# Optimization experiments

Measured on AMD Instinct MI355X. Metric: run time of the kernel, lower is better.

The kernel has to match this reference:

```python
import jax, jax.numpy as jnp
import numpy as np

NUM_CLASSES = 64
BASE_MARGIN = 0.1
ADAPTIVE_WEIGHT = 0.1
STAT_WEIGHT = 0.1


def setup_inputs() -> dict:
    key = jax.random.key(0)
    k1, k2 = jax.random.split(key)
    feats = jax.random.normal(k1, (4096, 512), dtype=jnp.float32)
    labels = jax.random.randint(k2, (4096,), 0, NUM_CLASSES, dtype=jnp.int64)
    return {"feats": feats, "labels": labels}


def _forward(feats, labels):
    N, D = feats.shape
    # pairwise euclidean distances (torch.cdist p=2), nan-safe sqrt
    sq = jnp.sum(feats * feats, axis=-1)                      # [N]
    d2 = sq[:, None] + sq[None, :] - 2.0 * (feats @ feats.T)  # [N,N]
    d2 = jnp.maximum(d2, 0.0)
    dist = jnp.sqrt(jnp.where(d2 > 0.0, d2, 1.0))
    dist = jnp.where(d2 > 0.0, dist, 0.0)

    # class stats (first-call EMA == batch stats), under stop_gradient (torch.no_grad)
    sg = jax.lax.stop_gradient(feats)
    counts = jax.ops.segment_sum(jnp.ones((N,), feats.dtype), labels, NUM_CLASSES)  # [C]
    denom = jnp.maximum(counts, 1.0)[:, None]
    cmean = jax.ops.segment_sum(sg, labels, NUM_CLASSES) / denom                    # [C,D]
    cmsq = jax.ops.segment_sum(sg * sg, labels, NUM_CLASSES) / denom                # [C,D]
    cvar = jnp.maximum(cmsq - cmean * cmean, 0.0)  # biased variance (unbiased=False)

    # statistical margin per sample: ||f_i - mean[y_i]|| * mean(var[y_i])
    diff = feats - cmean[labels]                               # grads flow via feats only
    center_dist2 = jnp.sum(diff * diff, axis=-1)
    center_dist = jnp.sqrt(jnp.where(center_dist2 > 0.0, center_dist2, 1.0))
    center_dist = jnp.where(center_dist2 > 0.0, center_dist, 0.0)
    uncertainty = jnp.mean(cvar, axis=-1)[labels]              # [N]
    stat_margin = center_dist * uncertainty

    same = labels[:, None] == labels[None, :]                  # [N,N]
    eye = jnp.eye(N, dtype=bool)
    pos_mask = same & ~eye                                     # matches pos_dist > 0 filter
    neg_mask = ~same

    big = jnp.asarray(1e30, dist.dtype)
    hardest_pos = jnp.max(jnp.where(pos_mask, dist, -big), axis=1)
    hardest_neg = jnp.min(jnp.where(neg_mask, dist, big), axis=1)
    pos_cnt = jnp.sum(pos_mask, axis=1).astype(dist.dtype)
    neg_cnt = jnp.sum(neg_mask, axis=1).astype(dist.dtype)
    mean_pos = jnp.sum(jnp.where(pos_mask, dist, 0.0), axis=1) / jnp.maximum(pos_cnt, 1.0)
    mean_neg = jnp.sum(jnp.where(neg_mask, dist, 0.0), axis=1) / jnp.maximum(neg_cnt, 1.0)

    final_margin = (BASE_MARGIN + ADAPTIVE_WEIGHT * (mean_neg - mean_pos)
                    + STAT_WEIGHT * stat_margin)
    per_sample = jax.nn.relu(hardest_pos - hardest_neg + final_margin)

    valid = (pos_cnt > 0) & (neg_cnt > 0)
    n_valid = jnp.sum(valid.astype(dist.dtype))
    loss = jnp.sum(jnp.where(valid, per_sample, 0.0)) / jnp.maximum(n_valid, 1.0)
    return jnp.where(n_valid > 0, loss, 0.0)


def reference(feats, labels):
    return _forward(feats, labels)
```

## Files before the change

### kernel.cpp

```cpp
#include <hip/hip_runtime.h>
#include <hip/hip_bf16.h>


#define NN 4096
#define DD 512
#define NCLS 64

typedef __bf16 bf16x8 __attribute__((ext_vector_type(8)));
typedef float f32x4 __attribute__((ext_vector_type(4)));

__device__ __forceinline__ void gload_lds16(const void* g, void* l) {
  __builtin_amdgcn_global_load_lds(
      (const __attribute__((address_space(1))) void*)g,
      (__attribute__((address_space(3))) void*)l, 16, 0, 0);
}

__global__ __launch_bounds__(512) void k_stats(
    const float* __restrict__ feats, const int* __restrict__ labels,
    float* __restrict__ counts, float* __restrict__ cmean,
    float* __restrict__ uncert) {
  __shared__ __align__(16) int slab[NN];
  __shared__ int list[NN];
  __shared__ int chunk_off[64];
  __shared__ int sM;
  __shared__ float sred[512];
  const int c = blockIdx.x;
  const int t = threadIdx.x;
  const int lane = t & 63;
  const int wv = t >> 6;
  for (int i = t; i < NN; i += 512) slab[i] = labels[i];
  __syncthreads();
  for (int ch = wv; ch < 64; ch += 8) {
    const unsigned long long m = __ballot(slab[ch * 64 + lane] == c);
    if (lane == 0) chunk_off[ch] = __popcll(m);
  }
  __syncthreads();
  if (wv == 0) {
    const int v = chunk_off[lane];
    int inc = v;
#pragma unroll
    for (int off = 1; off < 64; off <<= 1) {
      const int o = __shfl_up(inc, off);
      if (lane >= off) inc += o;
    }
    chunk_off[lane] = inc - v;
    if (lane == 63) sM = inc;
  }
  __syncthreads();
  const int M = sM;
  for (int ch = wv; ch < 64; ch += 8) {
    const bool my = (slab[ch * 64 + lane] == c);
    const unsigned long long m = __ballot(my);
    if (my) {
      const int pos = chunk_off[ch] + __popcll(m & ((1ULL << lane) - 1ULL));
      list[pos] = ch * 64 + lane;
    }
  }
  __syncthreads();
  float s1 = 0.f, s2 = 0.f;
  int m = 0;
  for (; m + 8 <= M; m += 8) {
    float v[8];
#pragma unroll
    for (int e = 0; e < 8; ++e) v[e] = feats[(size_t)list[m + e] * DD + t];
#pragma unroll
    for (int e = 0; e < 8; ++e) { s1 += v[e]; s2 += v[e] * v[e]; }
  }
  for (; m < M; ++m) {
    const float v = feats[(size_t)list[m] * DD + t];
    s1 += v; s2 += v * v;
  }
  const float den = fmaxf((float)M, 1.f);
  const float mean = s1 / den;
  const float var = fmaxf(s2 / den - mean * mean, 0.f);
  cmean[c * DD + t] = mean;
  sred[t] = var;
  __syncthreads();
  for (int s = 256; s > 0; s >>= 1) {
    if (t < s) sred[t] += sred[t + s];
    __syncthreads();
  }
  if (t == 0) {
    uncert[c] = sred[0] / (float)DD;
    counts[c] = (float)M;
  }
}

__global__ __launch_bounds__(256) void k_row(
    const float* __restrict__ feats, const int* __restrict__ labels,
    const float* __restrict__ cmean, unsigned short* __restrict__ fb,
    float* __restrict__ sqb, float* __restrict__ cd2) {
  const int w = threadIdx.x >> 6;
  const int lane = threadIdx.x & 63;
  const int row = blockIdx.x * 4 + w;
  const int lab = labels[row];
  const float4* fr = (const float4*)(feats + (size_t)row * DD);
  const float4* cm = (const float4*)(cmean + (size_t)lab * DD);
  float sq = 0.f, c2 = 0.f;
  unsigned int ob[4];
#pragma unroll
  for (int h = 0; h < 2; ++h) {
    const float4 f = fr[lane * 2 + h];
    const float4 cv = cm[lane * 2 + h];
    const float fe[4] = {f.x, f.y, f.z, f.w};
    const float ce[4] = {cv.x, cv.y, cv.z, cv.w};
    unsigned short us[4];
#pragma unroll
    for (int e = 0; e < 4; ++e) {
      const __bf16 b = (__bf16)fe[e];
      const float bf = (float)b;
      sq += bf * bf;
      const float dd = fe[e] - ce[e];
      c2 += dd * dd;
      us[e] = __builtin_bit_cast(unsigned short, b);
    }
    ob[h * 2]     = (unsigned int)us[0] | ((unsigned int)us[1] << 16);
    ob[h * 2 + 1] = (unsigned int)us[2] | ((unsigned int)us[3] << 16);
  }
  *(uint4*)(fb + (size_t)row * DD + lane * 8) = make_uint4(ob[0], ob[1], ob[2], ob[3]);
#pragma unroll
  for (int off = 32; off > 0; off >>= 1) {
    sq += __shfl_xor(sq, off);
    c2 += __shfl_xor(c2, off);
  }
  if (lane == 0) {
    sqb[row] = sq;
    cd2[row] = c2;
  }
}

__global__ __launch_bounds__(512, 2) void k_gemm(
    const unsigned short* __restrict__ fb, const float* __restrict__ sqb,
    const int* __restrict__ labels,
    float* __restrict__ php, float* __restrict__ phn,
    float* __restrict__ pst, float* __restrict__ pss) {
  __shared__ __align__(16) unsigned short sA[2][256 * 64];
  __shared__ __align__(16) unsigned short sB[2][256 * 64];
  __shared__ int s_labi[256], s_labj[256];
  __shared__ float s_sqi[256], s_sqj[256];

  const int bid = blockIdx.x;
  const int xcd = bid & 7;
  const int w8 = bid >> 3;
  const int ib = ((xcd & 3) << 2) + (w8 & 3);
  const int jb = ((xcd >> 2) << 3) + (w8 >> 2);
  const int ibase = ib << 8, jbase = jb << 8;
  const int t = threadIdx.x;
  const int lane = t & 63;
  const int w = t >> 6;
  const int wm = w >> 2;
  const int wn = w & 3;
  const int rin = lane & 15;
  const int g4 = lane >> 4;
  const int swzbyte = (g4 ^ (rin & 7)) << 4;
  const int abase = ((wm << 7) + rin) << 7;
  const int bbase = ((wn << 6) + rin) << 7;

  if (t < 256) {
    s_labi[t] = labels[ibase + t];
    s_labj[t] = labels[jbase + t];
    s_sqi[t] = sqb[ibase + t];
    s_sqj[t] = sqb[jbase + t];
  }

  const unsigned short* gA[4];
  const unsigned short* gB[4];
  int lo[4];
#pragma unroll
  for (int r = 0; r < 4; ++r) {
    const int q = (r << 9) + t;
    const int row = q >> 3;
    const int ch = q & 7;
    const int koff = (ch ^ (row & 7)) << 3;
    gA[r] = fb + (size_t)(ibase + row) * DD + koff;
    gB[r] = fb + (size_t)(jbase + row) * DD + koff;
    lo[r] = q << 3;
  }

  f32x4 acc[8][4];
#pragma unroll
  for (int mi = 0; mi < 8; ++mi)
#pragma unroll
    for (int nj = 0; nj < 4; ++nj)
      acc[mi][nj] = (f32x4){0.f, 0.f, 0.f, 0.f};

#pragma unroll
  for (int r = 0; r < 4; ++r) {
    gload_lds16(gA[r], &sA[0][lo[r]]);
    gload_lds16(gB[r], &sB[0][lo[r]]);
  }

#pragma unroll
  for (int kt = 0; kt < 8; ++kt) {
    const int cur = kt & 1;
    if (kt < 7) {
#pragma unroll
      for (int r = 0; r < 4; ++r) {
        gload_lds16(gA[r] + ((kt + 1) << 6), &sA[cur ^ 1][lo[r]]);
        gload_lds16(gB[r] + ((kt + 1) << 6), &sB[cur ^ 1][lo[r]]);
      }
      asm volatile("s_waitcnt vmcnt(8)" ::: "memory");
    } else {
      asm volatile("s_waitcnt vmcnt(0)" ::: "memory");
    }
    __builtin_amdgcn_s_barrier();
    const char* A = (const char*)sA[cur];
    const char* B = (const char*)sB[cur];
#pragma unroll
    for (int ks = 0; ks < 2; ++ks) {
      bf16x8 af[8], bg[4];
#pragma unroll
      for (int mi = 0; mi < 8; ++mi)
        af[mi] = *(const bf16x8*)(A + abase + (mi << 11) + (swzbyte ^ (ks << 6)));
#pragma unroll
      for (int nj = 0; nj < 4; ++nj)
        bg[nj] = *(const bf16x8*)(B + bbase + (nj << 11) + (swzbyte ^ (ks << 6)));
#pragma unroll
      for (int mi = 0; mi < 8; ++mi)
#pragma unroll
        for (int nj = 0; nj < 4; ++nj)
          acc[mi][nj] = __builtin_amdgcn_mfma_f32_16x16x32_bf16(
              af[mi], bg[nj], acc[mi][nj], 0, 0, 0);
    }
    if (kt < 7) {
      asm volatile("s_waitcnt lgkmcnt(0)" ::: "memory");
      __builtin_amdgcn_s_barrier();
    }
  }

  float qj[4];
  int lj[4];
#pragma unroll
  for (int nj = 0; nj < 4; ++nj) {
    const int cl = (wn << 6) + (nj << 4) + rin;
    qj[nj] = s_sqj[cl];
    lj[nj] = s_labj[cl];
  }
  const int jidx = (jb << 2) + wn;
#pragma unroll
  for (int mi = 0; mi < 8; ++mi) {
#pragma unroll
    for (int r = 0; r < 4; ++r) {
      const int rl = (wm << 7) + (mi << 4) + (g4 << 2) + r;
      const float qi = s_sqi[rl];
      const int li = s_labi[rl];
      float hp = 0.f, hn = 1e30f, st = 0.f, ss = 0.f;
#pragma unroll
      for (int nj = 0; nj < 4; ++nj) {
        const float g = acc[mi][nj][r];
        float d2 = qi + qj[nj] - 2.f * g;
        d2 = fmaxf(d2, 0.f);
        const float dist = sqrtf(d2);
        const bool same = (li == lj[nj]);
        const float dp = same ? dist : 0.f;
        hp = fmaxf(hp, dp);
        hn = fminf(hn, same ? 1e30f : dist);
        st += dist;
        ss += dp;
      }
#pragma unroll
      for (int off = 1; off < 16; off <<= 1) {
        hp = fmaxf(hp, __shfl_xor(hp, off));
        hn = fminf(hn, __shfl_xor(hn, off));
        st += __shfl_xor(st, off);
        ss += __shfl_xor(ss, off);
      }
      if (rin == 0) {
        const int grow = ibase + rl;
        php[jidx * NN + grow] = hp;
        phn[jidx * NN + grow] = hn;
        pst[jidx * NN + grow] = st;
        pss[jidx * NN + grow] = ss;
      }
    }
  }
}

__global__ __launch_bounds__(256) void k_fin1(
    const int* __restrict__ labels, const float* __restrict__ counts,
    const float* __restrict__ uncert, const float* __restrict__ cd2,
    const float* __restrict__ php, const float* __restrict__ phn,
    const float* __restrict__ pst, const float* __restrict__ pss,
    float* __restrict__ pf) {
  const int t = threadIdx.x;
  const int row = blockIdx.x * 256 + t;
  float hp = 0.f, hn = 1e30f, st = 0.f, ss = 0.f;
#pragma unroll 8
  for (int j = 0; j < 64; ++j) {
    hp = fmaxf(hp, php[j * NN + row]);
    hn = fminf(hn, phn[j * NN + row]);
    st += pst[j * NN + row];
    ss += pss[j * NN + row];
  }
  const int lab = labels[row];
  const float cnt = counts[lab];
  const float pos = cnt - 1.f;
  const float neg = (float)NN - cnt;
  const float mean_pos = ss / fmaxf(pos, 1.f);
  const float mean_neg = (st - ss) / fmaxf(neg, 1.f);
  const float c2 = cd2[row];
  const float cdist = (c2 > 0.f) ? sqrtf(c2) : 0.f;
  const float margin = 0.1f + 0.1f * (mean_neg - mean_pos) + 0.1f * (cdist * uncert[lab]);
  const float ps = fmaxf(hp - hn + margin, 0.f);
  const bool valid = (pos > 0.f) && (neg > 0.f);
  float s = valid ? ps : 0.f;
  float c = valid ? 1.f : 0.f;
#pragma unroll
  for (int off = 1; off < 64; off <<= 1) {
    s += __shfl_xor(s, off);
    c += __shfl_xor(c, off);
  }
  __shared__ float ws1[4], ws2[4];
  const int lane = t & 63;
  const int wv = t >> 6;
  if (lane == 0) { ws1[wv] = s; ws2[wv] = c; }
  __syncthreads();
  if (t == 0) {
    pf[2 * blockIdx.x] = ws1[0] + ws1[1] + ws1[2] + ws1[3];
    pf[2 * blockIdx.x + 1] = ws2[0] + ws2[1] + ws2[2] + ws2[3];
  }
}

__global__ __launch_bounds__(64) void k_fin2(const float* __restrict__ pf,
                                             float* __restrict__ out) {
  const int t = threadIdx.x;
  float s = 0.f, c = 0.f;
  if (t < 16) { s = pf[2 * t]; c = pf[2 * t + 1]; }
#pragma unroll
  for (int off = 1; off < 16; off <<= 1) {
    s += __shfl_xor(s, off);
    c += __shfl_xor(c, off);
  }
  if (t == 0) out[0] = (c > 0.f) ? (s / fmaxf(c, 1.f)) : 0.f;
}

extern "C" void kernel_launch(void* const* d_in, const int* in_sizes, int n_in,
                              void* d_out, int out_size, void* d_ws, size_t ws_size,
                              hipStream_t stream) {
  (void)in_sizes; (void)n_in; (void)out_size; (void)ws_size;
  const float* feats = (const float*)d_in[0];
  const int* labels = (const int*)d_in[1];
  char* w = (char*)d_ws;
  float* counts = (float*)(w + 0);
  float* uncert = (float*)(w + 1024);
  float* sqb    = (float*)(w + 2048);
  float* cd2    = (float*)(w + 18432);
  float* pf     = (float*)(w + 34816);
  float* cmean  = (float*)(w + 36864);
  unsigned short* fb = (unsigned short*)(w + 167936);
  float* php = (float*)(w + 4362240);
  float* phn = (float*)(w + 5410816);
  float* pst = (float*)(w + 6459392);
  float* pss = (float*)(w + 7507968);

  k_stats<<<dim3(64), dim3(512), 0, stream>>>(feats, labels, counts, cmean, uncert);
  k_row<<<dim3(1024), dim3(256), 0, stream>>>(feats, labels, cmean, fb, sqb, cd2);
  k_gemm<<<dim3(256), dim3(512), 0, stream>>>(fb, sqb, labels, php, phn, pst, pss);
  k_fin1<<<dim3(16), dim3(256), 0, stream>>>(labels, counts, uncert, cd2,
                                             php, phn, pst, pss, pf);
  k_fin2<<<dim3(1), dim3(64), 0, stream>>>(pf, (float*)d_out);
}
```

Before: 60.82 us.

## Interleave GEMM prefetch with split MFMA phases and parallelize final reduction

The GEMM main loop is restructured into four sub-phases per K tile. Each phase loads a half of the A fragments from LDS, issues a slice of the next tile's global-to-LDS prefetches, and runs its MFMA block under raised wave priority with barriers in between, in a ping-pong style schedule. This is meant to overlap memory traffic with matrix math and to reduce register pressure by holding only four A fragments at once; the two-blocks-per-CU launch bound is dropped. The final reduction kernel now uses 256 blocks with one wave per row and lane-wise loads across the 64 partials, replacing 16 blocks of strided per-thread loops, to improve parallelism and coalescing.

```diff
diff --git a/kernel.cpp b/kernel.cpp
--- a/kernel.cpp
+++ b/kernel.cpp
@@ -129,7 +129,7 @@
   }
 }
 
-__global__ __launch_bounds__(512, 2) void k_gemm(
+__global__ __launch_bounds__(512) void k_gemm(
     const unsigned short* __restrict__ fb, const float* __restrict__ sqb,
     const int* __restrict__ labels,
     float* __restrict__ php, float* __restrict__ phn,
@@ -189,43 +189,105 @@
     gload_lds16(gA[r], &sA[0][lo[r]]);
     gload_lds16(gB[r], &sB[0][lo[r]]);
   }
+  asm volatile("s_waitcnt vmcnt(0)" ::: "memory");
+  __builtin_amdgcn_s_barrier();
 
 #pragma unroll
   for (int kt = 0; kt < 8; ++kt) {
     const int cur = kt & 1;
-    if (kt < 7) {
-#pragma unroll
-      for (int r = 0; r < 4; ++r) {
-        gload_lds16(gA[r] + ((kt + 1) << 6), &sA[cur ^ 1][lo[r]]);
-        gload_lds16(gB[r] + ((kt + 1) << 6), &sB[cur ^ 1][lo[r]]);
-      }
-      asm volatile("s_waitcnt vmcnt(8)" ::: "memory");
-    } else {
-      asm volatile("s_waitcnt vmcnt(0)" ::: "memory");
-    }
-    __builtin_amdgcn_s_barrier();
     const char* A = (const char*)sA[cur];
     const char* B = (const char*)sB[cur];
-#pragma unroll
-    for (int ks = 0; ks < 2; ++ks) {
-      bf16x8 af[8], bg[4];
-#pragma unroll
-      for (int mi = 0; mi < 8; ++mi)
-        af[mi] = *(const bf16x8*)(A + abase + (mi << 11) + (swzbyte ^ (ks << 6)));
+    unsigned short* nA = sA[cur ^ 1];
+    unsigned short* nB = sB[cur ^ 1];
+    const int nk = (kt + 1) << 6;
+    bf16x8 af[4], bg[4];
+
+#pragma unroll
+    for (int mi = 0; mi < 4; ++mi)
+      af[mi] = *(const bf16x8*)(A + abase + (mi << 11) + swzbyte);
+#pragma unroll
+    for (int nj = 0; nj < 4; ++nj)
+      bg[nj] = *(const bf16x8*)(B + bbase + (nj << 11) + swzbyte);
+    if (kt < 7) {
+      gload_lds16(gA[0] + nk, &nA[lo[0]]);
+      gload_lds16(gA[1] + nk, &nA[lo[1]]);
+      gload_lds16(gA[2] + nk, &nA[lo[2]]);
+    }
+    __builtin_amdgcn_s_barrier();
+    asm volatile("s_waitcnt lgkmcnt(0)" ::: "memory");
+    __builtin_amdgcn_sched_barrier(0);
+    __builtin_amdgcn_s_setprio(1);
+#pragma unroll
+    for (int mi = 0; mi < 4; ++mi)
 #pragma unroll
       for (int nj = 0; nj < 4; ++nj)
-        bg[nj] = *(const bf16x8*)(B + bbase + (nj << 11) + (swzbyte ^ (ks << 6)));
-#pragma unroll
-      for (int mi = 0; mi < 8; ++mi)
-#pragma unroll
-        for (int nj = 0; nj < 4; ++nj)
-          acc[mi][nj] = __builtin_amdgcn_mfma_f32_16x16x32_bf16(
-              af[mi], bg[nj], acc[mi][nj], 0, 0, 0);
-    }
+        acc[mi][nj] = __builtin_amdgcn_mfma_f32_16x16x32_bf16(
+            af[mi], bg[nj], acc[mi][nj], 0, 0, 0);
+    __builtin_amdgcn_s_setprio(0);
+    __builtin_amdgcn_s_barrier();
+
+#pragma unroll
+    for (int mi = 0; mi < 4; ++mi)
+      af[mi] = *(const bf16x8*)(A + abase + ((mi + 4) << 11) + swzbyte);
     if (kt < 7) {
-      asm volatile("s_waitcnt lgkmcnt(0)" ::: "memory");
-      __builtin_amdgcn_s_barrier();
-    }
+      gload_lds16(gA[3] + nk, &nA[lo[3]]);
+      gload_lds16(gB[0] + nk, &nB[lo[0]]);
+      gload_lds16(gB[1] + nk, &nB[lo[1]]);
+    }
+    __builtin_amdgcn_s_barrier();
+    asm volatile("s_waitcnt lgkmcnt(0)" ::: "memory");
+    __builtin_amdgcn_sched_barrier(0);
+    __builtin_amdgcn_s_setprio(1);
+#pragma unroll
+    for (int mi = 0; mi < 4; ++mi)
+#pragma unroll
+      for (int nj = 0; nj < 4; ++nj)
+        acc[mi + 4][nj] = __builtin_amdgcn_mfma_f32_16x16x32_bf16(
+            af[mi], bg[nj], acc[mi + 4][nj], 0, 0, 0);
+    __builtin_amdgcn_s_setprio(0);
+    __builtin_amdgcn_s_barrier();
+
+#pragma unroll
+    for (int mi = 0; mi < 4; ++mi)
+      af[mi] = *(const bf16x8*)(A + abase + (mi << 11) + (swzbyte ^ 64));
+#pragma unroll
+    for (int nj = 0; nj < 4; ++nj)
+      bg[nj] = *(const bf16x8*)(B + bbase + (nj << 11) + (swzbyte ^ 64));
+    if (kt < 7) {
+      gload_lds16(gB[2] + nk, &nB[lo[2]]);
+      gload_lds16(gB[3] + nk, &nB[lo[3]]);
+    }
+    __builtin_amdgcn_s_barrier();
+    asm volatile("s_waitcnt lgkmcnt(0)" ::: "memory");
+    __builtin_amdgcn_sched_barrier(0);
+    __builtin_amdgcn_s_setprio(1);
+#pragma unroll
+    for (int mi = 0; mi < 4; ++mi)
+#pragma unroll
+      for (int nj = 0; nj < 4; ++nj)
+        acc[mi][nj] = __builtin_amdgcn_mfma_f32_16x16x32_bf16(
+            af[mi], bg[nj], acc[mi][nj], 0, 0, 0);
+    __builtin_amdgcn_s_setprio(0);
+    __builtin_amdgcn_s_barrier();
+
+#pragma unroll
+    for (int mi = 0; mi < 4; ++mi)
+      af[mi] = *(const bf16x8*)(A + abase + ((mi + 4) << 11) + (swzbyte ^ 64));
+    __builtin_amdgcn_s_barrier();
+    asm volatile("s_waitcnt lgkmcnt(0)" ::: "memory");
+    __builtin_amdgcn_sched_barrier(0);
+    __builtin_amdgcn_s_setprio(1);
+#pragma unroll
+    for (int mi = 0; mi < 4; ++mi)
+#pragma unroll
+      for (int nj = 0; nj < 4; ++nj)
+        acc[mi + 4][nj] = __builtin_amdgcn_mfma_f32_16x16x32_bf16(
+            af[mi], bg[nj], acc[mi + 4][nj], 0, 0, 0);
+    __builtin_amdgcn_s_setprio(0);
+    if (kt < 7) {
+      asm volatile("s_waitcnt vmcnt(0)" ::: "memory");
+    }
+    __builtin_amdgcn_s_barrier();
   }
 
   float qj[4];
@@ -276,62 +338,74 @@
   }
 }
 
-__global__ __launch_bounds__(256) void k_fin1(
+__global__ __launch_bounds__(1024) void k_fin1(
     const int* __restrict__ labels, const float* __restrict__ counts,
     const float* __restrict__ uncert, const float* __restrict__ cd2,
     const float* __restrict__ php, const float* __restrict__ phn,
     const float* __restrict__ pst, const float* __restrict__ pss,
     float* __restrict__ pf) {
   const int t = threadIdx.x;
-  const int row = blockIdx.x * 256 + t;
-  float hp = 0.f, hn = 1e30f, st = 0.f, ss = 0.f;
-#pragma unroll 8
-  for (int j = 0; j < 64; ++j) {
-    hp = fmaxf(hp, php[j * NN + row]);
-    hn = fminf(hn, phn[j * NN + row]);
-    st += pst[j * NN + row];
-    ss += pss[j * NN + row];
-  }
-  const int lab = labels[row];
-  const float cnt = counts[lab];
-  const float pos = cnt - 1.f;
-  const float neg = (float)NN - cnt;
-  const float mean_pos = ss / fmaxf(pos, 1.f);
-  const float mean_neg = (st - ss) / fmaxf(neg, 1.f);
-  const float c2 = cd2[row];
-  const float cdist = (c2 > 0.f) ? sqrtf(c2) : 0.f;
-  const float margin = 0.1f + 0.1f * (mean_neg - mean_pos) + 0.1f * (cdist * uncert[lab]);
-  const float ps = fmaxf(hp - hn + margin, 0.f);
-  const bool valid = (pos > 0.f) && (neg > 0.f);
-  float s = valid ? ps : 0.f;
-  float c = valid ? 1.f : 0.f;
+  const int wv = t >> 6;
+  const int lane = t & 63;
+  const int row = blockIdx.x * 16 + wv;
+  const size_t idx = (size_t)lane * NN + row;
+  float hp = php[idx];
+  float hn = phn[idx];
+  float st = pst[idx];
+  float ss = pss[idx];
+#pragma unroll
+  for (int off = 1; off < 64; off <<= 1) {
+    hp = fmaxf(hp, __shfl_xor(hp, off));
+    hn = fminf(hn, __shfl_xor(hn, off));
+    st += __shfl_xor(st, off);
+    ss += __shfl_xor(ss, off);
+  }
+  __shared__ float r1[16], r2[16];
+  if (lane == 0) {
+    const int lab = labels[row];
+    const float cnt = counts[lab];
+    const float pos = cnt - 1.f;
+    const float neg = (float)NN - cnt;
+    const float mean_pos = ss / fmaxf(pos, 1.f);
+    const float mean_neg = (st - ss) / fmaxf(neg, 1.f);
+    const float c2 = cd2[row];
+    const float cdist = (c2 > 0.f) ? sqrtf(c2) : 0.f;
+    const float margin = 0.1f + 0.1f * (mean_neg - mean_pos) + 0.1f * (cdist * uncert[lab]);
+    const float ps = fmaxf(hp - hn + margin, 0.f);
+    const bool valid = (pos > 0.f) && (neg > 0.f);
+    r1[wv] = valid ? ps : 0.f;
+    r2[wv] = valid ? 1.f : 0.f;
+  }
+  __syncthreads();
+  if (t == 0) {
+    float s = 0.f, c = 0.f;
+#pragma unroll
+    for (int k = 0; k < 16; ++k) { s += r1[k]; c += r2[k]; }
+    pf[2 * blockIdx.x] = s;
+    pf[2 * blockIdx.x + 1] = c;
+  }
+}
+
+__global__ __launch_bounds__(256) void k_fin2(const float* __restrict__ pf,
+                                              float* __restrict__ out) {
+  const int t = threadIdx.x;
+  const int lane = t & 63;
+  const int w = t >> 6;
+  float s = pf[2 * t];
+  float c = pf[2 * t + 1];
 #pragma unroll
   for (int off = 1; off < 64; off <<= 1) {
     s += __shfl_xor(s, off);
     c += __shfl_xor(c, off);
   }
   __shared__ float ws1[4], ws2[4];
-  const int lane = t & 63;
-  const int wv = t >> 6;
-  if (lane == 0) { ws1[wv] = s; ws2[wv] = c; }
+  if (lane == 0) { ws1[w] = s; ws2[w] = c; }
   __syncthreads();
   if (t == 0) {
-    pf[2 * blockIdx.x] = ws1[0] + ws1[1] + ws1[2] + ws1[3];
-    pf[2 * blockIdx.x + 1] = ws2[0] + ws2[1] + ws2[2] + ws2[3];
-  }
-}
-
-__global__ __launch_bounds__(64) void k_fin2(const float* __restrict__ pf,
-                                             float* __restrict__ out) {
-  const int t = threadIdx.x;
-  float s = 0.f, c = 0.f;
-  if (t < 16) { s = pf[2 * t]; c = pf[2 * t + 1]; }
-#pragma unroll
-  for (int off = 1; off < 16; off <<= 1) {
-    s += __shfl_xor(s, off);
-    c += __shfl_xor(c, off);
-  }
-  if (t == 0) out[0] = (c > 0.f) ? (s / fmaxf(c, 1.f)) : 0.f;
+    s = ws1[0] + ws1[1] + ws1[2] + ws1[3];
+    c = ws2[0] + ws2[1] + ws2[2] + ws2[3];
+    out[0] = (c > 0.f) ? (s / fmaxf(c, 1.f)) : 0.f;
+  }
 }
 
 extern "C" void kernel_launch(void* const* d_in, const int* in_sizes, int n_in,
@@ -356,7 +430,7 @@
   k_stats<<<dim3(64), dim3(512), 0, stream>>>(feats, labels, counts, cmean, uncert);
   k_row<<<dim3(1024), dim3(256), 0, stream>>>(feats, labels, cmean, fb, sqb, cd2);
   k_gemm<<<dim3(256), dim3(512), 0, stream>>>(fb, sqb, labels, php, phn, pst, pss);
-  k_fin1<<<dim3(16), dim3(256), 0, stream>>>(labels, counts, uncert, cd2,
-                                             php, phn, pst, pss, pf);
-  k_fin2<<<dim3(1), dim3(64), 0, stream>>>(pf, (float*)d_out);
-}
+  k_fin1<<<dim3(256), dim3(1024), 0, stream>>>(labels, counts, uncert, cd2,
+                                               php, phn, pst, pss, pf);
+  k_fin2<<<dim3(1), dim3(256), 0, stream>>>(pf, (float*)d_out);
+}
```

Result: no change. 60.54 us (-0.5%).

## Split class-stats and final reduction kernels across more blocks

Applied to the files above, without the earlier changes.

The class-statistics kernel now runs four blocks per class, each covering 128 feature dimensions, with four row-subgroups per block and a shared-memory combine. Per-part variance sums go to a small buffer that the finalize kernel adds up. The first finalize kernel changes from 16 blocks that loop serially over 64 partials to 256 blocks that use one wavefront per row and wave shuffles. The aim is to raise occupancy in the small, latency-bound kernels, at the cost of more redundant label scanning and list building per block.

```diff
diff --git a/kernel.cpp b/kernel.cpp
--- a/kernel.cpp
+++ b/kernel.cpp
@@ -18,13 +18,14 @@
 __global__ __launch_bounds__(512) void k_stats(
     const float* __restrict__ feats, const int* __restrict__ labels,
     float* __restrict__ counts, float* __restrict__ cmean,
-    float* __restrict__ uncert) {
+    float* __restrict__ pvar) {
   __shared__ __align__(16) int slab[NN];
   __shared__ int list[NN];
   __shared__ int chunk_off[64];
   __shared__ int sM;
-  __shared__ float sred[512];
-  const int c = blockIdx.x;
+  __shared__ float red1[512], red2[512];
+  const int c = blockIdx.x >> 2;
+  const int part = blockIdx.x & 3;
   const int t = threadIdx.x;
   const int lane = t & 63;
   const int wv = t >> 6;
@@ -57,32 +58,43 @@
     }
   }
   __syncthreads();
+  const int d = (part << 7) + (t & 127);
+  const int sub = t >> 7;
   float s1 = 0.f, s2 = 0.f;
-  int m = 0;
-  for (; m + 8 <= M; m += 8) {
-    float v[8];
-#pragma unroll
-    for (int e = 0; e < 8; ++e) v[e] = feats[(size_t)list[m + e] * DD + t];
-#pragma unroll
-    for (int e = 0; e < 8; ++e) { s1 += v[e]; s2 += v[e] * v[e]; }
-  }
-  for (; m < M; ++m) {
-    const float v = feats[(size_t)list[m] * DD + t];
+  int m = sub;
+  for (; m + 16 <= M; m += 16) {
+    float v[4];
+#pragma unroll
+    for (int e = 0; e < 4; ++e) v[e] = feats[(size_t)list[m + 4 * e] * DD + d];
+#pragma unroll
+    for (int e = 0; e < 4; ++e) { s1 += v[e]; s2 += v[e] * v[e]; }
+  }
+  for (; m < M; m += 4) {
+    const float v = feats[(size_t)list[m] * DD + d];
     s1 += v; s2 += v * v;
   }
-  const float den = fmaxf((float)M, 1.f);
-  const float mean = s1 / den;
-  const float var = fmaxf(s2 / den - mean * mean, 0.f);
-  cmean[c * DD + t] = mean;
-  sred[t] = var;
-  __syncthreads();
-  for (int s = 256; s > 0; s >>= 1) {
-    if (t < s) sred[t] += sred[t + s];
+  red1[t] = s1;
+  red2[t] = s2;
+  __syncthreads();
+  float var = 0.f;
+  if (t < 128) {
+    const float a1 = red1[t] + red1[t + 128] + red1[t + 256] + red1[t + 384];
+    const float a2 = red2[t] + red2[t + 128] + red2[t + 256] + red2[t + 384];
+    const float den = fmaxf((float)M, 1.f);
+    const float mean = a1 / den;
+    var = fmaxf(a2 / den - mean * mean, 0.f);
+    cmean[c * DD + d] = mean;
+  }
+  __syncthreads();
+  if (t < 128) red1[t] = var;
+  __syncthreads();
+  for (int s = 64; s > 0; s >>= 1) {
+    if (t < s) red1[t] += red1[t + s];
     __syncthreads();
   }
   if (t == 0) {
-    uncert[c] = sred[0] / (float)DD;
-    counts[c] = (float)M;
+    pvar[(c << 2) + part] = red1[0];
+    if (part == 0) counts[c] = (float)M;
   }
 }
 
@@ -276,62 +288,76 @@
   }
 }
 
-__global__ __launch_bounds__(256) void k_fin1(
+__global__ __launch_bounds__(1024) void k_fin1(
     const int* __restrict__ labels, const float* __restrict__ counts,
-    const float* __restrict__ uncert, const float* __restrict__ cd2,
+    const float* __restrict__ pvar, const float* __restrict__ cd2,
     const float* __restrict__ php, const float* __restrict__ phn,
     const float* __restrict__ pst, const float* __restrict__ pss,
     float* __restrict__ pf) {
   const int t = threadIdx.x;
-  const int row = blockIdx.x * 256 + t;
-  float hp = 0.f, hn = 1e30f, st = 0.f, ss = 0.f;
-#pragma unroll 8
-  for (int j = 0; j < 64; ++j) {
-    hp = fmaxf(hp, php[j * NN + row]);
-    hn = fminf(hn, phn[j * NN + row]);
-    st += pst[j * NN + row];
-    ss += pss[j * NN + row];
-  }
-  const int lab = labels[row];
-  const float cnt = counts[lab];
-  const float pos = cnt - 1.f;
-  const float neg = (float)NN - cnt;
-  const float mean_pos = ss / fmaxf(pos, 1.f);
-  const float mean_neg = (st - ss) / fmaxf(neg, 1.f);
-  const float c2 = cd2[row];
-  const float cdist = (c2 > 0.f) ? sqrtf(c2) : 0.f;
-  const float margin = 0.1f + 0.1f * (mean_neg - mean_pos) + 0.1f * (cdist * uncert[lab]);
-  const float ps = fmaxf(hp - hn + margin, 0.f);
-  const bool valid = (pos > 0.f) && (neg > 0.f);
-  float s = valid ? ps : 0.f;
-  float c = valid ? 1.f : 0.f;
+  const int wv = t >> 6;
+  const int lane = t & 63;
+  const int row = blockIdx.x * 16 + wv;
+  const size_t idx = (size_t)lane * NN + row;
+  float hp = php[idx];
+  float hn = phn[idx];
+  float st = pst[idx];
+  float ss = pss[idx];
+#pragma unroll
+  for (int off = 1; off < 64; off <<= 1) {
+    hp = fmaxf(hp, __shfl_xor(hp, off));
+    hn = fminf(hn, __shfl_xor(hn, off));
+    st += __shfl_xor(st, off);
+    ss += __shfl_xor(ss, off);
+  }
+  __shared__ float r1[16], r2[16];
+  if (lane == 0) {
+    const int lab = labels[row];
+    const float cnt = counts[lab];
+    const float pos = cnt - 1.f;
+    const float neg = (float)NN - cnt;
+    const float mean_pos = ss / fmaxf(pos, 1.f);
+    const float mean_neg = (st - ss) / fmaxf(neg, 1.f);
+    const float c2 = cd2[row];
+    const float cdist = (c2 > 0.f) ? sqrtf(c2) : 0.f;
+    const float uncert = (pvar[lab * 4] + pvar[lab * 4 + 1] +
+                          pvar[lab * 4 + 2] + pvar[lab * 4 + 3]) * (1.f / 512.f);
+    const float margin = 0.1f + 0.1f * (mean_neg - mean_pos) + 0.1f * (cdist * uncert);
+    const float ps = fmaxf(hp - hn + margin, 0.f);
+    const bool valid = (pos > 0.f) && (neg > 0.f);
+    r1[wv] = valid ? ps : 0.f;
+    r2[wv] = valid ? 1.f : 0.f;
+  }
+  __syncthreads();
+  if (t == 0) {
+    float s = 0.f, c = 0.f;
+#pragma unroll
+    for (int k = 0; k < 16; ++k) { s += r1[k]; c += r2[k]; }
+    pf[2 * blockIdx.x] = s;
+    pf[2 * blockIdx.x + 1] = c;
+  }
+}
+
+__global__ __launch_bounds__(256) void k_fin2(const float* __restrict__ pf,
+                                              float* __restrict__ out) {
+  const int t = threadIdx.x;
+  const int lane = t & 63;
+  const int w = t >> 6;
+  float s = pf[2 * t];
+  float c = pf[2 * t + 1];
 #pragma unroll
   for (int off = 1; off < 64; off <<= 1) {
     s += __shfl_xor(s, off);
     c += __shfl_xor(c, off);
   }
   __shared__ float ws1[4], ws2[4];
-  const int lane = t & 63;
-  const int wv = t >> 6;
-  if (lane == 0) { ws1[wv] = s; ws2[wv] = c; }
+  if (lane == 0) { ws1[w] = s; ws2[w] = c; }
   __syncthreads();
   if (t == 0) {
-    pf[2 * blockIdx.x] = ws1[0] + ws1[1] + ws1[2] + ws1[3];
-    pf[2 * blockIdx.x + 1] = ws2[0] + ws2[1] + ws2[2] + ws2[3];
-  }
-}
-
-__global__ __launch_bounds__(64) void k_fin2(const float* __restrict__ pf,
-                                             float* __restrict__ out) {
-  const int t = threadIdx.x;
-  float s = 0.f, c = 0.f;
-  if (t < 16) { s = pf[2 * t]; c = pf[2 * t + 1]; }
-#pragma unroll
-  for (int off = 1; off < 16; off <<= 1) {
-    s += __shfl_xor(s, off);
-    c += __shfl_xor(c, off);
-  }
-  if (t == 0) out[0] = (c > 0.f) ? (s / fmaxf(c, 1.f)) : 0.f;
+    s = ws1[0] + ws1[1] + ws1[2] + ws1[3];
+    c = ws2[0] + ws2[1] + ws2[2] + ws2[3];
+    out[0] = (c > 0.f) ? (s / fmaxf(c, 1.f)) : 0.f;
+  }
 }
 
 extern "C" void kernel_launch(void* const* d_in, const int* in_sizes, int n_in,
@@ -342,7 +368,7 @@
   const int* labels = (const int*)d_in[1];
   char* w = (char*)d_ws;
   float* counts = (float*)(w + 0);
-  float* uncert = (float*)(w + 1024);
+  float* pvar   = (float*)(w + 1024);
   float* sqb    = (float*)(w + 2048);
   float* cd2    = (float*)(w + 18432);
   float* pf     = (float*)(w + 34816);
@@ -353,10 +379,10 @@
   float* pst = (float*)(w + 6459392);
   float* pss = (float*)(w + 7507968);
 
-  k_stats<<<dim3(64), dim3(512), 0, stream>>>(feats, labels, counts, cmean, uncert);
+  k_stats<<<dim3(256), dim3(512), 0, stream>>>(feats, labels, counts, cmean, pvar);
   k_row<<<dim3(1024), dim3(256), 0, stream>>>(feats, labels, cmean, fb, sqb, cd2);
   k_gemm<<<dim3(256), dim3(512), 0, stream>>>(fb, sqb, labels, php, phn, pst, pss);
-  k_fin1<<<dim3(16), dim3(256), 0, stream>>>(labels, counts, uncert, cd2,
-                                             php, phn, pst, pss, pf);
-  k_fin2<<<dim3(1), dim3(64), 0, stream>>>(pf, (float*)d_out);
-}
+  k_fin1<<<dim3(256), dim3(1024), 0, stream>>>(labels, counts, pvar, cd2,
+                                               php, phn, pst, pss, pf);
+  k_fin2<<<dim3(1), dim3(256), 0, stream>>>(pf, (float*)d_out);
+}
```

Measured after the change: 58.36 us. 1.04x faster.
